# Optimization experiments

Hardware: AMD Instinct MI355X
Metric: run time of the kernel (lower is better)

The kernel has to match this reference:

```python
import jax, jax.numpy as jnp
import numpy as np

N, DIM, HID, E = 100000, 128, 512, 600000


def setup_inputs() -> dict:
    key = jax.random.key(0)
    k_h, k_src, k_dst, k_w1, k_b1, k_w2, k_b2 = jax.random.split(key, 7)
    h = jax.random.normal(k_h, (N, DIM), dtype=jnp.float32)
    src = jax.random.randint(k_src, (E,), 0, N)
    dst = jax.random.randint(k_dst, (E,), 0, N)
    edge_index = jnp.stack([src, dst], axis=0).astype(jnp.int64)
    # Linear params stored as [in, out] (math-equivalent to torch's [out,in].T)
    s1 = 1.0 / np.sqrt(2 * DIM)
    s2 = 1.0 / np.sqrt(HID)
    W1 = jax.random.uniform(k_w1, (2 * DIM, HID), jnp.float32, -s1, s1)
    b1 = jax.random.uniform(k_b1, (HID,), jnp.float32, -s1, s1)
    W2 = jax.random.uniform(k_w2, (HID, DIM), jnp.float32, -s2, s2)
    b2 = jax.random.uniform(k_b2, (DIM,), jnp.float32, -s2, s2)
    return {"h": h, "edge_index": edge_index, "W1": W1, "b1": b1, "W2": W2, "b2": b2}


def reference(h, edge_index, W1, b1, W2, b2):
    src, dst = edge_index[0], edge_index[1]
    n = h.shape[0]
    # scatter-mean: sum gathered neighbor features per destination node
    agg_sum = jax.ops.segment_sum(h[src], dst, num_segments=n)  # [N, DIM]
    deg = jax.ops.segment_sum(jnp.ones((src.shape[0],), h.dtype), dst, num_segments=n)  # [N]
    mean = agg_sum / jnp.maximum(deg, 1.0)[:, None]
    # isolated nodes (deg==0) fall back to their own features
    agg = jnp.where((deg == 0)[:, None], h, mean)
    x = jnp.concatenate([h, agg], axis=-1)  # [N, 2*DIM]
    hdn = jax.nn.gelu(x @ W1 + b1, approximate=False)  # torch GELU default = exact erf
    return hdn @ W2 + b2
```

## Files before the change

### kernel.cpp

```cpp
#include <hip/hip_runtime.h>
#include <hip/hip_bf16.h>
#include <math.h>

#define N_NODES 100000
#define DIM 128
#define HID 512
#define EDGES 600000
#define SCAN_CHUNK 1024
#define SCAN_NBLK ((N_NODES + SCAN_CHUNK - 1) / SCAN_CHUNK)
#define MROWS_PAD 100096

typedef short bf16x8 __attribute__((ext_vector_type(8)));
typedef float f32x4 __attribute__((ext_vector_type(4)));


__device__ inline unsigned short f32_to_bf16(float f) {
    unsigned int u = __float_as_uint(f);
    u += 0x7fff + ((u >> 16) & 1);
    return (unsigned short)(u >> 16);
}

__device__ inline float gelu_f(float x) {
    float x3 = x * x * x;
    float y = 0.7978845608028654f * x + 0.0356774081f * x3;
    float e = exp2f(y * 2.8853900817779268f);
    float t = 1.0f - 2.0f * __builtin_amdgcn_rcpf(e + 1.0f);
    return 0.5f * x * (1.0f + t);
}

__device__ inline void gload16(const void* g, void* l) {
    __builtin_amdgcn_global_load_lds(
        (const __attribute__((address_space(1))) unsigned int*)g,
        (__attribute__((address_space(3))) unsigned int*)l,
        16, 0, 0);
}

#define PREP_W1_BLKS 512
#define PREP_W2_BLKS 128
#define PREP_CONV_BLKS 12500
#define PREP_COUNT_BLKS ((EDGES + 255) / 256)
#define PREP_TOTAL (PREP_W1_BLKS + PREP_W2_BLKS + PREP_CONV_BLKS + PREP_COUNT_BLKS)

__global__ __launch_bounds__(256) void mgl_prep_kernel(
    const float* __restrict__ h, const int* __restrict__ ei,
    const float* __restrict__ W1, const float* __restrict__ W2,
    unsigned short* __restrict__ X, unsigned short* __restrict__ W1T,
    unsigned short* __restrict__ W2T, int* __restrict__ cnt)
{
    int b = blockIdx.x;
    if (b < PREP_W1_BLKS) {
        int n = b;
        int k = threadIdx.x;
        unsigned short val = f32_to_bf16(W1[(size_t)k * HID + n]);
        int byteoff = (k * 2) ^ ((n & 7) << 4);
        *(unsigned short*)((char*)(W1T + (size_t)n * 256) + byteoff) = val;
        return;
    }
    b -= PREP_W1_BLKS;
    if (b < PREP_W2_BLKS) {
        int n = b;
        #pragma unroll
        for (int it = 0; it < 2; ++it) {
            int k = threadIdx.x + it * 256;
            unsigned short val = f32_to_bf16(W2[(size_t)k * DIM + n]);
            int byteoff = (k * 2) ^ ((n & 7) << 4);
            *(unsigned short*)((char*)(W2T + (size_t)n * 512) + byteoff) = val;
        }
        return;
    }
    b -= PREP_W2_BLKS;
    if (b < PREP_CONV_BLKS) {
        int t = b * 256 + threadIdx.x;
        if (t >= N_NODES * (DIM / 4)) return;
        int node = t >> 5;
        int c4 = t & 31;
        float4 v = *(const float4*)(h + (size_t)node * DIM + c4 * 4);
        ushort4 p;
        p.x = f32_to_bf16(v.x); p.y = f32_to_bf16(v.y);
        p.z = f32_to_bf16(v.z); p.w = f32_to_bf16(v.w);
        int byteoff = (c4 * 8) ^ ((node & 7) << 4);
        *(ushort4*)((char*)(X + (size_t)node * 256) + byteoff) = p;
        return;
    }
    b -= PREP_CONV_BLKS;
    {
        int e = b * 256 + threadIdx.x;
        if (e < EDGES) atomicAdd(&cnt[ei[EDGES + e]], 1);
    }
}

__global__ __launch_bounds__(256) void mgl_scan_block_kernel(
    const int* __restrict__ cnt, int* __restrict__ row_start, int* __restrict__ bsum)
{
    __shared__ int sdata[256];
    int t = threadIdx.x;
    int base = blockIdx.x * SCAN_CHUNK + t * 4;
    int v[4];
    #pragma unroll
    for (int i = 0; i < 4; ++i) {
        int idx = base + i;
        v[i] = (idx < N_NODES) ? cnt[idx] : 0;
    }
    int tsum = v[0] + v[1] + v[2] + v[3];
    sdata[t] = tsum;
    __syncthreads();
    for (int off = 1; off < 256; off <<= 1) {
        int x = (t >= off) ? sdata[t - off] : 0;
        __syncthreads();
        sdata[t] += x;
        __syncthreads();
    }
    int run = (t > 0) ? sdata[t - 1] : 0;
    #pragma unroll
    for (int i = 0; i < 4; ++i) {
        int idx = base + i;
        if (idx < N_NODES) row_start[idx] = run;
        run += v[i];
    }
    if (t == 255) bsum[blockIdx.x] = sdata[255];
}

__global__ __launch_bounds__(128) void mgl_scan_bsum_kernel(int* __restrict__ bsum)
{
    __shared__ int sd[128];
    int t = threadIdx.x;
    int v = (t < SCAN_NBLK) ? bsum[t] : 0;
    sd[t] = v;
    __syncthreads();
    for (int off = 1; off < 128; off <<= 1) {
        int x = (t >= off) ? sd[t - off] : 0;
        __syncthreads();
        sd[t] += x;
        __syncthreads();
    }
    if (t < SCAN_NBLK) bsum[t] = sd[t] - v;
}

__global__ __launch_bounds__(256) void mgl_scan_add_kernel(
    int* __restrict__ row_start, const int* __restrict__ bsum)
{
    int i = blockIdx.x * 256 + threadIdx.x;
    if (i < N_NODES) row_start[i] += bsum[i / SCAN_CHUNK];
    if (i == 0) row_start[N_NODES] = EDGES;
}

__global__ __launch_bounds__(256) void mgl_fill_kernel(
    const int* __restrict__ ei, const int* __restrict__ row_start,
    int* __restrict__ cnt, int* __restrict__ csr)
{
    int e = blockIdx.x * 256 + threadIdx.x;
    if (e >= EDGES) return;
    int s = ei[e];
    int t = ei[EDGES + e];
    int pos = atomicSub(&cnt[t], 1) - 1;
    csr[row_start[t] + pos] = s;
}

__global__ __launch_bounds__(256) void mgl_gather_mean_kernel(
    const unsigned short* __restrict__ Xb, const int* __restrict__ row_start,
    const int* __restrict__ csr, unsigned short* __restrict__ X)
{
    int v = blockIdx.x * 4 + (threadIdx.x >> 6);
    if (v >= N_NODES) return;
    int lane = threadIdx.x & 63;
    int beg = row_start[v];
    int nb = row_start[v + 1] - beg;
    int laneByte = lane * 4;
    const char* xb = (const char*)Xb;

    if (nb > 0) {
        float2 acc = make_float2(0.f, 0.f);
        for (int base = 0; base < nb; base += 64) {
            int rem = nb - base; if (rem > 64) rem = 64;
            int sv = (lane < rem) ? csr[beg + base + lane] : 0;
            for (int j = 0; j < rem; ++j) {
                int s = __shfl(sv, j);
                unsigned int pk = *(const unsigned int*)(
                    xb + (size_t)s * 512 + (laneByte ^ ((s & 7) << 4)));
                acc.x += __uint_as_float(pk << 16);
                acc.y += __uint_as_float(pk & 0xffff0000u);
            }
        }
        float inv = 1.f / (float)nb;
        unsigned int po = (unsigned int)f32_to_bf16(acc.x * inv) |
                          ((unsigned int)f32_to_bf16(acc.y * inv) << 16);
        *(unsigned int*)((char*)(X + (size_t)v * 256) +
                         ((256 + laneByte) ^ ((v & 7) << 4))) = po;
    } else {
        unsigned int pk = *(const unsigned int*)(
            xb + (size_t)v * 512 + (laneByte ^ ((v & 7) << 4)));
        *(unsigned int*)((char*)(X + (size_t)v * 256) +
                         ((256 + laneByte) ^ ((v & 7) << 4))) = pk;
    }
}

__global__ __launch_bounds__(512, 4) void mgl_fused_mlp_kernel(
    const unsigned short* __restrict__ W1T,
    const unsigned short* __restrict__ W2T,
    const unsigned short* __restrict__ Xr,
    const float* __restrict__ b1f, const float* __restrict__ b2f,
    float* __restrict__ outp)
{
    __shared__ char lds[65536];
    char* W1l = lds;
    char* W2l = lds + 32768;
    const int tid = threadIdx.x;
    const int w = tid >> 6, l = tid & 63;
    const int r16 = l & 15, kq = l >> 4;
    const int rmask = (r16 & 7) << 4;
    char* bnc = lds + 49152 + w * 2048;

    const size_t m0 = (size_t)blockIdx.x * 128;
    const size_t m = m0 + w * 16 + r16;

    bf16x8 xf[8];
    {
        const char* xrow = (const char*)Xr + m * 512;
        int swz = ((int)m & 7) << 4;
        #pragma unroll
        for (int ks = 0; ks < 8; ++ks)
            xf[ks] = *(const bf16x8*)(xrow + ((ks * 64 + kq * 16) ^ swz));
    }

    f32x4 acc[8] = {};

    for (int t = 0; t < 8; ++t) {
        {
            const char* src = (const char*)W1T + (size_t)t * 32768;
            #pragma unroll
            for (int i = 0; i < 4; ++i) {
                int off = i * 8192 + tid * 16;
                gload16(src + off, W1l + off);
            }
        }
        {
            #pragma unroll
            for (int i = 0; i < 2; ++i) {
                int p = tid + i * 512;
                int o = p >> 3, c16 = (p & 7) * 16;
                const char* src = (const char*)W2T + (size_t)o * 1024 + t * 128 + c16;
                gload16(src, W2l + o * 128 + c16);
            }
        }
        __syncthreads();

        #pragma unroll
        for (int ni = 0; ni < 4; ++ni) {
            f32x4 s = {};
            #pragma unroll
            for (int ks = 0; ks < 8; ++ks) {
                bf16x8 a = *(const bf16x8*)(W1l + (ni * 16 + r16) * 512 +
                                            ((ks * 64 + kq * 16) ^ rmask));
                s = __builtin_amdgcn_mfma_f32_16x16x32_bf16(a, xf[ks], s, 0, 0, 0);
            }
            float4 bv = *(const float4*)(b1f + t * 64 + ni * 16 + kq * 4);
            float g0 = gelu_f(s[0] + bv.x);
            float g1 = gelu_f(s[1] + bv.y);
            float g2 = gelu_f(s[2] + bv.z);
            float g3 = gelu_f(s[3] + bv.w);
            uint2 pk;
            pk.x = (unsigned int)f32_to_bf16(g0) | ((unsigned int)f32_to_bf16(g1) << 16);
            pk.y = (unsigned int)f32_to_bf16(g2) | ((unsigned int)f32_to_bf16(g3) << 16);
            *(uint2*)(bnc + r16 * 128 + ((ni * 32 + kq * 8) ^ rmask)) = pk;
        }

        #pragma unroll
        for (int c = 0; c < 2; ++c) {
            bf16x8 b = *(const bf16x8*)(bnc + r16 * 128 + ((c * 64 + kq * 16) ^ rmask));
            #pragma unroll
            for (int oi = 0; oi < 8; ++oi) {
                bf16x8 a = *(const bf16x8*)(W2l + (oi * 16 + r16) * 128 +
                                            ((c * 64 + kq * 16) ^ rmask));
                acc[oi] = __builtin_amdgcn_mfma_f32_16x16x32_bf16(a, b, acc[oi], 0, 0, 0);
            }
        }
        __syncthreads();
    }

    if (m < N_NODES) {
        float* orow = outp + m * DIM;
        #pragma unroll
        for (int oi = 0; oi < 8; ++oi) {
            float4 bv = *(const float4*)(b2f + oi * 16 + kq * 4);
            float4 o;
            o.x = acc[oi][0] + bv.x;
            o.y = acc[oi][1] + bv.y;
            o.z = acc[oi][2] + bv.z;
            o.w = acc[oi][3] + bv.w;
            *(float4*)(orow + oi * 16 + kq * 4) = o;
        }
    }
}

extern "C" void kernel_launch(void* const* d_in, const int* in_sizes, int n_in,
                              void* d_out, int out_size, void* d_ws, size_t ws_size,
                              hipStream_t stream) {
    const float* h  = (const float*)d_in[0];
    const int*   ei = (const int*)d_in[1];
    const float* W1 = (const float*)d_in[2];
    const float* b1 = (const float*)d_in[3];
    const float* W2 = (const float*)d_in[4];
    const float* b2 = (const float*)d_in[5];
    float* out = (float*)d_out;

    unsigned short* X   = (unsigned short*)d_ws;
    unsigned short* W1T = X + (size_t)MROWS_PAD * 256;
    unsigned short* W2T = W1T + 512 * 256;
    int* cnt = (int*)(W2T + 128 * 512);
    int* row_start = cnt + N_NODES;
    int* bsum = row_start + N_NODES + 1;
    int* csr = bsum + 128;

    hipMemsetAsync(cnt, 0, N_NODES * sizeof(int), stream);
    mgl_prep_kernel<<<PREP_TOTAL, 256, 0, stream>>>(h, ei, W1, W2, X, W1T, W2T, cnt);
    mgl_scan_block_kernel<<<SCAN_NBLK, 256, 0, stream>>>(cnt, row_start, bsum);
    mgl_scan_bsum_kernel<<<1, 128, 0, stream>>>(bsum);
    mgl_scan_add_kernel<<<(N_NODES + 255) / 256, 256, 0, stream>>>(row_start, bsum);
    mgl_fill_kernel<<<(EDGES + 255) / 256, 256, 0, stream>>>(ei, row_start, cnt, csr);
    mgl_gather_mean_kernel<<<(N_NODES + 3) / 4, 256, 0, stream>>>(X, row_start, csr, X);

    mgl_fused_mlp_kernel<<<MROWS_PAD / 128, 512, 0, stream>>>(
        W1T, W2T, X, b1, b2, out);
}
```

Baseline: 234.4 us.

## Give each MLP wave two 16-row tiles to reuse weight fragments from LDS

The fused MLP kernel moves from 8 waves of 16 rows each to 4 waves of 32 rows each. Every W1 and W2 fragment read from LDS now feeds two MFMAs, which halves LDS read traffic per FLOP and gives more independent MFMA chains. The cost is more registers (two X fragment sets and doubled accumulators), a larger per-wave GELU scratch area, and half as many threads to load weights. Launch bounds drop to 256 threads with 2 blocks per CU, which may lower occupancy.

```diff
diff --git a/kernel.cpp b/kernel.cpp
--- a/kernel.cpp
+++ b/kernel.cpp
@@ -194,7 +194,7 @@
     }
 }
 
-__global__ __launch_bounds__(512, 4) void mgl_fused_mlp_kernel(
+__global__ __launch_bounds__(256, 2) void mgl_fused_mlp_kernel(
     const unsigned short* __restrict__ W1T,
     const unsigned short* __restrict__ W2T,
     const unsigned short* __restrict__ Xr,
@@ -208,35 +208,36 @@
     const int w = tid >> 6, l = tid & 63;
     const int r16 = l & 15, kq = l >> 4;
     const int rmask = (r16 & 7) << 4;
-    char* bnc = lds + 49152 + w * 2048;
+    char* bnc = lds + 49152 + w * 4096;
 
     const size_t m0 = (size_t)blockIdx.x * 128;
-    const size_t m = m0 + w * 16 + r16;
-
-    bf16x8 xf[8];
-    {
+
+    bf16x8 xf[2][8];
+    #pragma unroll
+    for (int mi = 0; mi < 2; ++mi) {
+        size_t m = m0 + w * 32 + mi * 16 + r16;
         const char* xrow = (const char*)Xr + m * 512;
         int swz = ((int)m & 7) << 4;
         #pragma unroll
         for (int ks = 0; ks < 8; ++ks)
-            xf[ks] = *(const bf16x8*)(xrow + ((ks * 64 + kq * 16) ^ swz));
-    }
-
-    f32x4 acc[8] = {};
+            xf[mi][ks] = *(const bf16x8*)(xrow + ((ks * 64 + kq * 16) ^ swz));
+    }
+
+    f32x4 acc[2][8] = {};
 
     for (int t = 0; t < 8; ++t) {
         {
             const char* src = (const char*)W1T + (size_t)t * 32768;
             #pragma unroll
-            for (int i = 0; i < 4; ++i) {
-                int off = i * 8192 + tid * 16;
+            for (int i = 0; i < 8; ++i) {
+                int off = i * 4096 + tid * 16;
                 gload16(src + off, W1l + off);
             }
         }
         {
             #pragma unroll
-            for (int i = 0; i < 2; ++i) {
-                int p = tid + i * 512;
+            for (int i = 0; i < 4; ++i) {
+                int p = tid + i * 256;
                 int o = p >> 3, c16 = (p & 7) * 16;
                 const char* src = (const char*)W2T + (size_t)o * 1024 + t * 128 + c16;
                 gload16(src, W2l + o * 128 + c16);
@@ -246,47 +247,57 @@
 
         #pragma unroll
         for (int ni = 0; ni < 4; ++ni) {
-            f32x4 s = {};
+            f32x4 s0 = {}, s1 = {};
             #pragma unroll
             for (int ks = 0; ks < 8; ++ks) {
                 bf16x8 a = *(const bf16x8*)(W1l + (ni * 16 + r16) * 512 +
                                             ((ks * 64 + kq * 16) ^ rmask));
-                s = __builtin_amdgcn_mfma_f32_16x16x32_bf16(a, xf[ks], s, 0, 0, 0);
+                s0 = __builtin_amdgcn_mfma_f32_16x16x32_bf16(a, xf[0][ks], s0, 0, 0, 0);
+                s1 = __builtin_amdgcn_mfma_f32_16x16x32_bf16(a, xf[1][ks], s1, 0, 0, 0);
             }
             float4 bv = *(const float4*)(b1f + t * 64 + ni * 16 + kq * 4);
-            float g0 = gelu_f(s[0] + bv.x);
-            float g1 = gelu_f(s[1] + bv.y);
-            float g2 = gelu_f(s[2] + bv.z);
-            float g3 = gelu_f(s[3] + bv.w);
-            uint2 pk;
-            pk.x = (unsigned int)f32_to_bf16(g0) | ((unsigned int)f32_to_bf16(g1) << 16);
-            pk.y = (unsigned int)f32_to_bf16(g2) | ((unsigned int)f32_to_bf16(g3) << 16);
-            *(uint2*)(bnc + r16 * 128 + ((ni * 32 + kq * 8) ^ rmask)) = pk;
+            uint2 pk0, pk1;
+            pk0.x = (unsigned int)f32_to_bf16(gelu_f(s0[0] + bv.x)) |
+                    ((unsigned int)f32_to_bf16(gelu_f(s0[1] + bv.y)) << 16);
+            pk0.y = (unsigned int)f32_to_bf16(gelu_f(s0[2] + bv.z)) |
+                    ((unsigned int)f32_to_bf16(gelu_f(s0[3] + bv.w)) << 16);
+            pk1.x = (unsigned int)f32_to_bf16(gelu_f(s1[0] + bv.x)) |
+                    ((unsigned int)f32_to_bf16(gelu_f(s1[1] + bv.y)) << 16);
+            pk1.y = (unsigned int)f32_to_bf16(gelu_f(s1[2] + bv.z)) |
+                    ((unsigned int)f32_to_bf16(gelu_f(s1[3] + bv.w)) << 16);
+            int colb = (ni * 32 + kq * 8) ^ rmask;
+            *(uint2*)(bnc + r16 * 128 + colb) = pk0;
+            *(uint2*)(bnc + (16 + r16) * 128 + colb) = pk1;
         }
 
         #pragma unroll
         for (int c = 0; c < 2; ++c) {
-            bf16x8 b = *(const bf16x8*)(bnc + r16 * 128 + ((c * 64 + kq * 16) ^ rmask));
+            int colb = (c * 64 + kq * 16) ^ rmask;
+            bf16x8 b0 = *(const bf16x8*)(bnc + r16 * 128 + colb);
+            bf16x8 b1 = *(const bf16x8*)(bnc + (16 + r16) * 128 + colb);
             #pragma unroll
             for (int oi = 0; oi < 8; ++oi) {
-                bf16x8 a = *(const bf16x8*)(W2l + (oi * 16 + r16) * 128 +
-                                            ((c * 64 + kq * 16) ^ rmask));
-                acc[oi] = __builtin_amdgcn_mfma_f32_16x16x32_bf16(a, b, acc[oi], 0, 0, 0);
-            }
-        }
-        __syncthreads();
-    }
-
-    if (m < N_NODES) {
+                bf16x8 a = *(const bf16x8*)(W2l + (oi * 16 + r16) * 128 + colb);
+                acc[0][oi] = __builtin_amdgcn_mfma_f32_16x16x32_bf16(a, b0, acc[0][oi], 0, 0, 0);
+                acc[1][oi] = __builtin_amdgcn_mfma_f32_16x16x32_bf16(a, b1, acc[1][oi], 0, 0, 0);
+            }
+        }
+        __syncthreads();
+    }
+
+    #pragma unroll
+    for (int mi = 0; mi < 2; ++mi) {
+        size_t m = m0 + w * 32 + mi * 16 + r16;
+        if (m >= N_NODES) continue;
         float* orow = outp + m * DIM;
         #pragma unroll
         for (int oi = 0; oi < 8; ++oi) {
             float4 bv = *(const float4*)(b2f + oi * 16 + kq * 4);
             float4 o;
-            o.x = acc[oi][0] + bv.x;
-            o.y = acc[oi][1] + bv.y;
-            o.z = acc[oi][2] + bv.z;
-            o.w = acc[oi][3] + bv.w;
+            o.x = acc[mi][oi][0] + bv.x;
+            o.y = acc[mi][oi][1] + bv.y;
+            o.z = acc[mi][oi][2] + bv.z;
+            o.w = acc[mi][oi][3] + bv.w;
             *(float4*)(orow + oi * 16 + kq * 4) = o;
         }
     }
@@ -319,6 +330,6 @@
     mgl_fill_kernel<<<(EDGES + 255) / 256, 256, 0, stream>>>(ei, row_start, cnt, csr);
     mgl_gather_mean_kernel<<<(N_NODES + 3) / 4, 256, 0, stream>>>(X, row_start, csr, X);
 
-    mgl_fused_mlp_kernel<<<MROWS_PAD / 128, 512, 0, stream>>>(
+    mgl_fused_mlp_kernel<<<MROWS_PAD / 128, 256, 0, stream>>>(
         W1T, W2T, X, b1, b2, out);
 }
```

Result: slower. 240.3 us (+2.5%).
